# Kernel tuning notes

Measured on AMD Instinct MI355X. Metric: run time of the kernel, lower is better.

Reference implementation:

```python
import jax, jax.numpy as jnp
import numpy as np
import math

B, T, C = 4, 1024, 2048
NH, HS = 16, 128          # n_head, head_size
NLQ, NLKV = 512, 512      # q_latent_dim, kv_latent_dim
DHR = 64                  # rope_head_dim


def setup_inputs() -> dict:
    key = jax.random.key(0)
    ks = jax.random.split(key, 10)
    def w(k, shape, fan_in):
        return jax.random.normal(k, shape, jnp.float32) * (1.0 / math.sqrt(fan_in))
    # RoPE frequencies (standard theta=10000), (T, DHR//2)
    half = DHR // 2
    inv_freq = 1.0 / (10000.0 ** (np.arange(0, half, dtype=np.float32) * 2.0 / DHR))
    ang = np.arange(T, dtype=np.float32)[:, None] * inv_freq[None, :]
    return {
        "x":     jax.random.normal(ks[0], (B, T, C), jnp.float32),
        "W_dq":  w(ks[1], (NLQ, C), C),
        "W_uq":  w(ks[2], (C, NLQ), NLQ),
        "W_dkv": w(ks[3], (NLKV, C), C),
        "W_uk":  w(ks[4], (C, NLKV), NLKV),
        "W_uv":  w(ks[5], (C, NLKV), NLKV),
        "W_o":   w(ks[6], (C, C), C),
        "W_qr":  w(ks[7], (NH * DHR, NLQ), NLQ),
        "W_kr":  w(ks[8], (DHR, C), C),
        "freqs_cos": jnp.asarray(np.cos(ang)),
        "freqs_sin": jnp.asarray(np.sin(ang)),
    }


def _rope(x, cos, sin):
    # x: (B, T, H, D); cos/sin: (T, D//2). Rotate pairs (even, odd).
    b, t, h, d = x.shape
    x_ = x.reshape(b, t, h, d // 2, 2)
    re, im = x_[..., 0], x_[..., 1]
    cos = cos[None, :, None, :]
    sin = sin[None, :, None, :]
    out = jnp.stack([re * cos - im * sin, re * sin + im * cos], axis=-1)
    return out.reshape(b, t, h, d)


def reference(x, W_dq, W_uq, W_dkv, W_uk, W_uv, W_o, W_qr, W_kr, freqs_cos, freqs_sin):
    # Absorbed matrices (training path, rope):
    # k_eff: (nh, nlq, hs) @ (nh, hs, nlkv) -> (nh, nlq, nlkv)
    k_eff = jnp.einsum('hqd,hdk->hqk',
                       W_uq.reshape(NLQ, NH, HS).transpose(1, 0, 2),
                       W_uk.reshape(NH, HS, NLKV))
    # v_eff: (W_uv.T @ W_o.T) -> (nlkv, nh, hs) -> (nh, nlkv, hs)
    v_eff = (W_uv.T @ W_o.T).reshape(NLKV, NH, HS).transpose(1, 0, 2)

    c_kv = x @ W_dkv.T          # (B, T, nlkv)
    c_q = x @ W_dq.T            # (B, T, nlq)

    # content logits: (B, nh, T, T)
    tmp = jnp.einsum('btq,hqk->bhtk', c_q, k_eff)
    attn_c = jnp.einsum('bhtk,bsk->bhts', tmp, c_kv)

    # rope logits
    c_kr = (x @ W_kr.T)[:, :, None, :]                       # (B, T, 1, dhr)
    k_r = _rope(c_kr, freqs_cos, freqs_sin)[:, :, 0, :]      # (B, T, dhr)
    c_qr = (c_q @ W_qr.T).reshape(B, T, NH, DHR)
    q_r = _rope(c_qr, freqs_cos, freqs_sin)                  # (B, T, nh, dhr)
    attn_r = jnp.einsum('bthd,bsd->bhts', q_r, k_r)

    scale = 1.0 / math.sqrt(HS + DHR)
    logits = (attn_c + attn_r) * scale
    causal = jnp.arange(T)[:, None] >= jnp.arange(T)[None, :]
    logits = jnp.where(causal[None, None], logits, -jnp.inf)
    attn = jax.nn.softmax(logits, axis=-1)

    y = jnp.einsum('bhts,bsk->bhtk', attn, c_kv)
    y = jnp.einsum('bhtk,hkd->bthd', y, v_eff).reshape(B, T, C)
    return y
```

## Files before the change

kernel.cpp:

```cpp
#include <hip/hip_runtime.h>
#include <hip/hip_bf16.h>

typedef __attribute__((ext_vector_type(8))) short short8;
typedef __attribute__((ext_vector_type(4))) float f32x4;
typedef __hip_bfloat16 bf16;

#define MFMA16(a,b,c) __builtin_amdgcn_mfma_f32_16x16x32_bf16(a,b,c,0,0,0)

__device__ __forceinline__ void gld_lds16(const void* g, void* l) {
  __builtin_amdgcn_global_load_lds((const __attribute__((address_space(1))) void*)g,
                                   (__attribute__((address_space(3))) void*)l, 16, 0, 0);
}


__global__ __launch_bounds__(256) void cast_bf16_kernel(const float* __restrict__ in,
                                                        bf16* __restrict__ out, long n4) {
  long i = (long)blockIdx.x * blockDim.x + threadIdx.x;
  if (i >= n4) return;
  float4 v = ((const float4*)in)[i];
  union { bf16 b[4]; uint2 u; } p;
  p.b[0] = __float2bfloat16(v.x);
  p.b[1] = __float2bfloat16(v.y);
  p.b[2] = __float2bfloat16(v.z);
  p.b[3] = __float2bfloat16(v.w);
  ((uint2*)out)[i] = p.u;
}

__global__ void transpose_cast_kernel(const float* __restrict__ in, bf16* __restrict__ out,
                                      int R, int C) {
  __shared__ float t[32][33];
  int c0 = blockIdx.x * 32, r0 = blockIdx.y * 32;
  for (int j = threadIdx.y; j < 32; j += 8)
    t[j][threadIdx.x] = in[(long)(r0 + j) * C + c0 + threadIdx.x];
  __syncthreads();
  for (int j = threadIdx.y; j < 32; j += 8)
    out[(long)(c0 + j) * R + r0 + threadIdx.x] = __float2bfloat16(t[threadIdx.x][j]);
}

__global__ __launch_bounds__(256) void rope_q_kernel(const float* __restrict__ in,
                                                     const float* __restrict__ cosT,
                                                     const float* __restrict__ sinT,
                                                     bf16* __restrict__ out, long total) {
  long i = (long)blockIdx.x * blockDim.x + threadIdx.x;
  if (i >= total) return;
  int pair = (int)(i & 31);
  long rest = i >> 5;
  int h = (int)(rest & 15);
  long bt = rest >> 4;
  int t = (int)(bt & 1023);
  long base = (bt * 16 + h) * 64 + pair * 2;
  float re = in[base], im = in[base + 1];
  float c = cosT[t * 32 + pair], s = sinT[t * 32 + pair];
  out[base] = __float2bfloat16(re * c - im * s);
  out[base + 1] = __float2bfloat16(re * s + im * c);
}

__global__ __launch_bounds__(256) void rope_k_kernel(const bf16* __restrict__ ckv_all,
                                                     const float* __restrict__ cosT,
                                                     const float* __restrict__ sinT,
                                                     bf16* __restrict__ out, long total) {
  long i = (long)blockIdx.x * blockDim.x + threadIdx.x;
  if (i >= total) return;
  int pair = (int)(i & 31);
  long bt = i >> 5;
  int t = (int)(bt & 1023);
  const bf16* src = ckv_all + bt * 1088 + 1024 + pair * 2;
  float re = __bfloat162float(src[0]), im = __bfloat162float(src[1]);
  float c = cosT[t * 32 + pair], s = sinT[t * 32 + pair];
  out[bt * 64 + pair * 2] = __float2bfloat16(re * c - im * s);
  out[bt * 64 + pair * 2 + 1] = __float2bfloat16(re * s + im * c);
}

template <int OUT>
__global__ __launch_bounds__(256) void gemm_nt(const bf16* __restrict__ A,
                                               const bf16* __restrict__ B,
                                               void* __restrict__ Cv, int M, int N, int K,
                                               int lda, int ldb, int ldc,
                                               int adiv, int amod, long astr,
                                               int bdiv, int bmod, long bstr, long cstr) {
  __shared__ bf16 As[128 * 32];
  __shared__ bf16 Bs[128 * 32];
  const int tid = threadIdx.x;
  const int lane = tid & 63;
  const int w = tid >> 6;
  const int wr = w >> 1, wc = w & 1;
  const int z = blockIdx.z;
  A += ((long)((z / adiv) % amod)) * astr;
  B += ((long)((z / bdiv) % bmod)) * bstr;
  const int m0 = blockIdx.x * 128, n0 = blockIdx.y * 128;
  const int l16 = lane & 15, lg = lane >> 4;
  const int r0c = tid >> 2, c8 = (tid & 3) * 8;
  f32x4 acc[4][4] = {};
  for (int k0 = 0; k0 < K; k0 += 32) {
    __syncthreads();
    gld_lds16(A + (long)(m0 + r0c) * lda + k0 + c8, &As[tid * 8]);
    gld_lds16(A + (long)(m0 + 64 + r0c) * lda + k0 + c8, &As[2048 + tid * 8]);
    gld_lds16(B + (long)(n0 + r0c) * ldb + k0 + c8, &Bs[tid * 8]);
    gld_lds16(B + (long)(n0 + 64 + r0c) * ldb + k0 + c8, &Bs[2048 + tid * 8]);
    __syncthreads();
    short8 af[4], bfr[4];
#pragma unroll
    for (int i = 0; i < 4; ++i) {
      af[i] = *(const short8*)(&As[(wr * 64 + i * 16 + l16) * 32 + lg * 8]);
      bfr[i] = *(const short8*)(&Bs[(wc * 64 + i * 16 + l16) * 32 + lg * 8]);
    }
#pragma unroll
    for (int i = 0; i < 4; ++i)
#pragma unroll
      for (int j2 = 0; j2 < 4; ++j2) acc[i][j2] = MFMA16(af[i], bfr[j2], acc[i][j2]);
  }
#pragma unroll
  for (int i = 0; i < 4; ++i)
#pragma unroll
    for (int j2 = 0; j2 < 4; ++j2) {
      int col = n0 + wc * 64 + j2 * 16 + l16;
      if (col >= N) continue;
      long rbase = (long)(m0 + wr * 64 + i * 16 + lg * 4);
      for (int r = 0; r < 4; ++r) {
        float v = acc[i][j2][r];
        long idx = (long)z * cstr + (rbase + r) * ldc + col;
        if (OUT == 1) ((bf16*)Cv)[idx] = __float2bfloat16(v);
        else if (OUT == 0) ((float*)Cv)[idx] = v;
        else atomicAdd(&((float*)Cv)[idx], v);
      }
    }
}

__global__ __launch_bounds__(512, 4) void attn_kernel(const bf16* __restrict__ q_h,
                                                      const bf16* __restrict__ q_r,
                                                      const bf16* __restrict__ kh,
                                                      const bf16* __restrict__ kr,
                                                      const bf16* __restrict__ vT,
                                                      float* __restrict__ out) {
  const int x = blockIdx.x, h = blockIdx.y, b = blockIdx.z;
  const int tid = threadIdx.x, lane = tid & 63, w = tid >> 6;
  const int l16 = lane & 15, lg = lane >> 4;
  __shared__ bf16 Klds[2][32 * 192];
  __shared__ bf16 Vlds[2][512 * 8];
  __shared__ bf16 Plds[8][16][40];

  const float sc = 0.0721687836f * 1.44269504f;
  const bf16* vbase = vT + (long)(b * 16 + h) * 131072;
  const int swz = l16 & 7;
  const int vswz = (l16 >> 1) & 3;

  int krow[2], kcs[2];
#pragma unroll
  for (int j = 0; j < 2; ++j) {
    int chunk = tid + 512 * j;
    int row = chunk / 24, c = chunk % 24;
    krow[j] = row & 31;
    kcs[j] = c ^ (row & 7);
  }
  const int vd = tid >> 2, vch = (tid & 3) ^ ((tid >> 3) & 3);

  for (int half = 0; half < 2; ++half) {
    const int q = half ? x : (7 - x);
    const int t0 = q * 128;
    const int rowmin = t0 + w * 16;
    const int nt = (t0 + 128) >> 5;

    short8 aq[6];
    {
      const int trow = t0 + w * 16 + l16;
      const bf16* qhp = q_h + ((long)(b * 1024 + trow)) * 2048 + h * 128;
#pragma unroll
      for (int kk = 0; kk < 4; ++kk) aq[kk] = *(const short8*)(qhp + kk * 32 + lg * 8);
      const bf16* qrp = q_r + (((long)b * 1024 + trow) * 16 + h) * 64;
      aq[4] = *(const short8*)(qrp + lg * 8);
      aq[5] = *(const short8*)(qrp + 32 + lg * 8);
    }

    f32x4 oacc[8] = {};
    float m_run[4], l_run[4];
#pragma unroll
    for (int r = 0; r < 4; ++r) { m_run[r] = -1e30f; l_run[r] = 0.f; }

    const bf16* ksrc[2];
    int kstep[2];
#pragma unroll
    for (int j = 0; j < 2; ++j) {
      if (kcs[j] < 16) { ksrc[j] = kh + ((long)b * 1024 + krow[j]) * 2048 + h * 128 + kcs[j] * 8; kstep[j] = 32 * 2048; }
      else             { ksrc[j] = kr + ((long)b * 1024 + krow[j]) * 64 + (kcs[j] - 16) * 8; kstep[j] = 32 * 64; }
    }
    const bf16* vsrc = vbase + (long)vd * 1024 + vch * 8;

    auto STAGE = [&](int cc) {
      gld_lds16(ksrc[0], &Klds[cc][tid * 8]);
      ksrc[0] += kstep[0];
      if (tid < 256) {
        gld_lds16(ksrc[1], &Klds[cc][(tid + 512) * 8]);
        ksrc[1] += kstep[1];
      }
      gld_lds16(vsrc, &Vlds[cc][tid * 8]);
      vsrc += 32;
    };

    int cur = 0;
    STAGE(0);
    __syncthreads();

    for (int t = 0; t < nt; ++t) {
      if (t + 1 < nt) STAGE(cur ^ 1);
      const int s0 = t * 32;
      if (s0 < rowmin + 16) {
        const bf16* Kb = &Klds[cur][0];
        f32x4 s_acc[2] = {};
#pragma unroll
        for (int kk = 0; kk < 6; ++kk) {
          int u = kk * 4 + lg;
          short8 b0 = *(const short8*)(Kb + l16 * 192 + ((u ^ swz) * 8));
          short8 b1 = *(const short8*)(Kb + (16 + l16) * 192 + ((u ^ swz) * 8));
          s_acc[0] = MFMA16(aq[kk], b0, s_acc[0]);
          s_acc[1] = MFMA16(aq[kk], b1, s_acc[1]);
        }
        const bool need_mask = (s0 + 31 > rowmin);
        float p[2][4], rmax[4];
#pragma unroll
        for (int r = 0; r < 4; ++r) {
          float s0v = s_acc[0][r] * sc, s1v = s_acc[1][r] * sc;
          if (need_mask) {
            int tg = rowmin + lg * 4 + r;
            if (s0 + l16 > tg) s0v = -1e30f;
            if (s0 + 16 + l16 > tg) s1v = -1e30f;
          }
          p[0][r] = s0v; p[1][r] = s1v;
          float mx = fmaxf(s0v, s1v);
          mx = fmaxf(mx, __shfl_xor(mx, 1));
          mx = fmaxf(mx, __shfl_xor(mx, 2));
          mx = fmaxf(mx, __shfl_xor(mx, 4));
          mx = fmaxf(mx, __shfl_xor(mx, 8));
          rmax[r] = mx;
        }
        float need = rmax[0] - m_run[0];
        need = fmaxf(need, rmax[1] - m_run[1]);
        need = fmaxf(need, rmax[2] - m_run[2]);
        need = fmaxf(need, rmax[3] - m_run[3]);
        if (__any(need > 8.0f)) {
          float alpha[4];
#pragma unroll
          for (int r = 0; r < 4; ++r) {
            float mnew = fmaxf(m_run[r], rmax[r]);
            alpha[r] = exp2f(m_run[r] - mnew);
            m_run[r] = mnew;
            l_run[r] *= alpha[r];
          }
#pragma unroll
          for (int f = 0; f < 8; ++f)
#pragma unroll
            for (int r = 0; r < 4; ++r) oacc[f][r] *= alpha[r];
        }
#pragma unroll
        for (int r = 0; r < 4; ++r) {
          float p0 = exp2f(p[0][r] - m_run[r]);
          float p1 = exp2f(p[1][r] - m_run[r]);
          p[0][r] = p0; p[1][r] = p1;
          float rs = p0 + p1;
          rs += __shfl_xor(rs, 1);
          rs += __shfl_xor(rs, 2);
          rs += __shfl_xor(rs, 4);
          rs += __shfl_xor(rs, 8);
          l_run[r] += rs;
        }
#pragma unroll
        for (int nf = 0; nf < 2; ++nf)
#pragma unroll
          for (int r = 0; r < 4; ++r)
            Plds[w][lg * 4 + r][nf * 16 + l16] = __float2bfloat16(p[nf][r]);
        short8 pa = *(const short8*)(&Plds[w][l16][lg * 8]);
        const bf16* Vb = &Vlds[cur][0];
#pragma unroll
        for (int f = 0; f < 8; ++f) {
          int slot = (f * 16 + l16) * 4 + (lg ^ vswz);
          short8 vb = *(const short8*)(Vb + slot * 8);
          oacc[f] = MFMA16(pa, vb, oacc[f]);
        }
      }
      __syncthreads();
      cur ^= 1;
    }

#pragma unroll
    for (int f = 0; f < 8; ++f)
#pragma unroll
      for (int r = 0; r < 4; ++r) {
        int t = t0 + w * 16 + lg * 4 + r;
        int col = f * 16 + l16;
        out[((long)(b * 1024 + t)) * 2048 + h * 128 + col] = oacc[f][r] / l_run[r];
      }
  }
}

extern "C" void kernel_launch(void* const* d_in, const int* in_sizes, int n_in, void* d_out,
                              int out_size, void* d_ws, size_t ws_size, hipStream_t stream) {
  const float* x = (const float*)d_in[0];
  const float* W_dq = (const float*)d_in[1];
  const float* W_uq = (const float*)d_in[2];
  const float* W_dkv = (const float*)d_in[3];
  const float* W_uk = (const float*)d_in[4];
  const float* W_uv = (const float*)d_in[5];
  const float* W_o = (const float*)d_in[6];
  const float* W_qr = (const float*)d_in[7];
  const float* W_kr = (const float*)d_in[8];
  const float* fcos = (const float*)d_in[9];
  const float* fsin = (const float*)d_in[10];
  float* out = (float*)d_out;

  char* p = (char*)d_ws;
  auto alloc = [&](long bytes) { void* r = p; p += (bytes + 255) & ~255L; return r; };
  bf16* xb = (bf16*)alloc(8388608L * 2);
  bf16* Wcat = (bf16*)alloc(1152L * 2048 * 2);
  bf16* Wqr_b = (bf16*)alloc(524288L * 2);
  bf16* Wo_b = (bf16*)alloc(4194304L * 2);
  bf16* Wcat2 = (bf16*)alloc(2097152L * 2);
  bf16* WuvT_b = (bf16*)alloc(1048576L * 2);
  bf16* ckv_all = (bf16*)alloc(4096L * 1088 * 2);
  float* veff_f32 = (float*)alloc(1048576L * 4);
  bf16* veffT_b = (bf16*)alloc(1048576L * 2);
  bf16* q_h = (bf16*)alloc(8388608L * 2);
  bf16* k_h = (bf16*)alloc(8388608L * 2);
  float* c_qr_f = (float*)alloc(4194304L * 4);
  bf16* q_r_b = (bf16*)alloc(4194304L * 2);
  bf16* k_r_b = (bf16*)alloc(262144L * 2);
  bf16* vT_b = (bf16*)alloc(8388608L * 2);
  bf16* WuqT_b = Wcat2;
  bf16* Wuk_b = Wcat2 + 1048576L;

  cast_bf16_kernel<<<8192, 256, 0, stream>>>(x, xb, 2097152);
  cast_bf16_kernel<<<1024, 256, 0, stream>>>(W_dq, Wcat, 262144);
  cast_bf16_kernel<<<1024, 256, 0, stream>>>(W_dkv, Wcat + 512L * 2048, 262144);
  cast_bf16_kernel<<<128, 256, 0, stream>>>(W_kr, Wcat + 1024L * 2048, 32768);
  cast_bf16_kernel<<<512, 256, 0, stream>>>(W_qr, Wqr_b, 131072);
  cast_bf16_kernel<<<4096, 256, 0, stream>>>(W_o, Wo_b, 1048576);
  cast_bf16_kernel<<<1024, 256, 0, stream>>>(W_uk, Wuk_b, 262144);
  transpose_cast_kernel<<<dim3(64, 16), dim3(32, 8), 0, stream>>>(W_uq, WuqT_b, 512, 2048);
  transpose_cast_kernel<<<dim3(16, 64), dim3(32, 8), 0, stream>>>(W_uv, WuvT_b, 2048, 512);
  hipMemsetAsync(veff_f32, 0, 1048576L * 4, stream);

  gemm_nt<1><<<dim3(32, 9, 1), 256, 0, stream>>>(xb, Wcat, ckv_all, 4096, 1088, 2048, 2048, 2048,
                                                 1088, 1, 1, 0, 1, 1, 0, 0);
  gemm_nt<2><<<dim3(16, 4, 4), 256, 0, stream>>>(Wo_b, WuvT_b, veff_f32, 2048, 512, 512, 2048,
                                                 2048, 512, 1, 4, 512, 1, 4, 512, 0);
  cast_bf16_kernel<<<1024, 256, 0, stream>>>(veff_f32, veffT_b, 262144);
  gemm_nt<1><<<dim3(32, 16, 2), 256, 0, stream>>>(ckv_all, Wcat2, q_h, 4096, 2048, 512, 1088,
                                                  512, 2048, 1, 2, 512, 1, 2, 1048576, 8388608);
  gemm_nt<0><<<dim3(32, 8, 1), 256, 0, stream>>>(ckv_all, Wqr_b, c_qr_f, 4096, 1024, 512, 1088,
                                                 512, 1024, 1, 1, 0, 1, 1, 0, 0);
  gemm_nt<1><<<dim3(1, 8, 64), 256, 0, stream>>>(veffT_b, ckv_all + 512, vT_b, 128, 1024, 512,
                                                 512, 1088, 1024, 1, 16, 65536, 16, 4,
                                                 1024L * 1088, 131072);
  rope_q_kernel<<<8192, 256, 0, stream>>>(c_qr_f, fcos, fsin, q_r_b, 2097152);
  rope_k_kernel<<<512, 256, 0, stream>>>(ckv_all, fcos, fsin, k_r_b, 131072);
  attn_kernel<<<dim3(4, 16, 4), 512, 0, stream>>>(q_h, q_r_b, k_h, k_r_b, vT_b, out);
}
```

Baseline: 390.4 us.

## Add 256x256 GEMM for q/k absorption, bf16 c_qr, one query block per attention CTA

Replaces the q_h/k_h absorbed-projection GEMM with a new 256x256-tile, 512-thread bf16 GEMM that gives each wave more output reuse. The c_qr intermediate is now written and read as bf16 instead of fp32, which halves that buffer's traffic at the cost of an extra rounding before RoPE. The attention kernel now launches one CTA per 128-row query block (largest first) instead of pairing a long and a short block in one CTA, which gives more CTAs but a less even amount of work per CTA. The new GEMM has a single LDS buffer with no prefetch and assumes the dimensions divide evenly.

```diff
diff --git a/kernel.cpp b/kernel.cpp
--- a/kernel.cpp
+++ b/kernel.cpp
@@ -37,7 +37,7 @@
     out[(long)(c0 + j) * R + r0 + threadIdx.x] = __float2bfloat16(t[threadIdx.x][j]);
 }
 
-__global__ __launch_bounds__(256) void rope_q_kernel(const float* __restrict__ in,
+__global__ __launch_bounds__(256) void rope_q_kernel(const bf16* __restrict__ in,
                                                      const float* __restrict__ cosT,
                                                      const float* __restrict__ sinT,
                                                      bf16* __restrict__ out, long total) {
@@ -49,7 +49,7 @@
   long bt = rest >> 4;
   int t = (int)(bt & 1023);
   long base = (bt * 16 + h) * 64 + pair * 2;
-  float re = in[base], im = in[base + 1];
+  float re = __bfloat162float(in[base]), im = __bfloat162float(in[base + 1]);
   float c = cosT[t * 32 + pair], s = sinT[t * 32 + pair];
   out[base] = __float2bfloat16(re * c - im * s);
   out[base + 1] = __float2bfloat16(re * s + im * c);
@@ -126,13 +126,68 @@
     }
 }
 
+__global__ __launch_bounds__(512) void gemm256_nt(const bf16* __restrict__ A,
+                                                  const bf16* __restrict__ B,
+                                                  bf16* __restrict__ C, int K,
+                                                  int lda, int ldb, int ldc,
+                                                  long astr, long bstr, long cstr) {
+  __shared__ bf16 As[256 * 32];
+  __shared__ bf16 Bs[256 * 32];
+  const int tid = threadIdx.x;
+  const int lane = tid & 63;
+  const int w = tid >> 6;
+  const int wr = w >> 2, wc = w & 3;
+  const int z = blockIdx.z;
+  A += (long)z * astr;
+  B += (long)z * bstr;
+  C += (long)z * cstr;
+  const int m0 = blockIdx.x * 256, n0 = blockIdx.y * 256;
+  const int l16 = lane & 15, lg = lane >> 4;
+  const int r0 = tid >> 2, c0 = tid & 3;
+  const int cs0 = c0 ^ (r0 & 3);
+  const int r1 = 128 + r0, cs1 = c0 ^ (r1 & 3);
+  const int swz = l16 & 3;
+  f32x4 acc[8][4] = {};
+  for (int k0 = 0; k0 < K; k0 += 32) {
+    __syncthreads();
+    gld_lds16(A + (long)(m0 + r0) * lda + k0 + cs0 * 8, &As[tid * 8]);
+    gld_lds16(A + (long)(m0 + r1) * lda + k0 + cs1 * 8, &As[(tid + 512) * 8]);
+    gld_lds16(B + (long)(n0 + r0) * ldb + k0 + cs0 * 8, &Bs[tid * 8]);
+    gld_lds16(B + (long)(n0 + r1) * ldb + k0 + cs1 * 8, &Bs[(tid + 512) * 8]);
+    __syncthreads();
+    short8 bfr[4];
+#pragma unroll
+    for (int j = 0; j < 4; ++j) {
+      int row = wc * 64 + j * 16 + l16;
+      bfr[j] = *(const short8*)(&Bs[(row * 4 + (lg ^ swz)) * 8]);
+    }
+#pragma unroll
+    for (int i = 0; i < 8; ++i) {
+      int row = wr * 128 + i * 16 + l16;
+      short8 af = *(const short8*)(&As[(row * 4 + (lg ^ swz)) * 8]);
+#pragma unroll
+      for (int j = 0; j < 4; ++j) acc[i][j] = MFMA16(af, bfr[j], acc[i][j]);
+    }
+  }
+#pragma unroll
+  for (int i = 0; i < 8; ++i)
+#pragma unroll
+    for (int j = 0; j < 4; ++j) {
+      int col = n0 + wc * 64 + j * 16 + l16;
+      long rbase = (long)(m0 + wr * 128 + i * 16 + lg * 4);
+#pragma unroll
+      for (int r = 0; r < 4; ++r)
+        C[(rbase + r) * (long)ldc + col] = __float2bfloat16(acc[i][j][r]);
+    }
+}
+
 __global__ __launch_bounds__(512, 4) void attn_kernel(const bf16* __restrict__ q_h,
                                                       const bf16* __restrict__ q_r,
                                                       const bf16* __restrict__ kh,
                                                       const bf16* __restrict__ kr,
                                                       const bf16* __restrict__ vT,
                                                       float* __restrict__ out) {
-  const int x = blockIdx.x, h = blockIdx.y, b = blockIdx.z;
+  const int qb = 7 - blockIdx.x, h = blockIdx.y, b = blockIdx.z;
   const int tid = threadIdx.x, lane = tid & 63, w = tid >> 6;
   const int l16 = lane & 15, lg = lane >> 4;
   __shared__ bf16 Klds[2][32 * 192];
@@ -154,141 +209,138 @@
   }
   const int vd = tid >> 2, vch = (tid & 3) ^ ((tid >> 3) & 3);
 
-  for (int half = 0; half < 2; ++half) {
-    const int q = half ? x : (7 - x);
-    const int t0 = q * 128;
-    const int rowmin = t0 + w * 16;
-    const int nt = (t0 + 128) >> 5;
-
-    short8 aq[6];
-    {
-      const int trow = t0 + w * 16 + l16;
-      const bf16* qhp = q_h + ((long)(b * 1024 + trow)) * 2048 + h * 128;
-#pragma unroll
-      for (int kk = 0; kk < 4; ++kk) aq[kk] = *(const short8*)(qhp + kk * 32 + lg * 8);
-      const bf16* qrp = q_r + (((long)b * 1024 + trow) * 16 + h) * 64;
-      aq[4] = *(const short8*)(qrp + lg * 8);
-      aq[5] = *(const short8*)(qrp + 32 + lg * 8);
-    }
-
-    f32x4 oacc[8] = {};
-    float m_run[4], l_run[4];
-#pragma unroll
-    for (int r = 0; r < 4; ++r) { m_run[r] = -1e30f; l_run[r] = 0.f; }
-
-    const bf16* ksrc[2];
-    int kstep[2];
-#pragma unroll
-    for (int j = 0; j < 2; ++j) {
-      if (kcs[j] < 16) { ksrc[j] = kh + ((long)b * 1024 + krow[j]) * 2048 + h * 128 + kcs[j] * 8; kstep[j] = 32 * 2048; }
-      else             { ksrc[j] = kr + ((long)b * 1024 + krow[j]) * 64 + (kcs[j] - 16) * 8; kstep[j] = 32 * 64; }
-    }
-    const bf16* vsrc = vbase + (long)vd * 1024 + vch * 8;
-
-    auto STAGE = [&](int cc) {
-      gld_lds16(ksrc[0], &Klds[cc][tid * 8]);
-      ksrc[0] += kstep[0];
-      if (tid < 256) {
-        gld_lds16(ksrc[1], &Klds[cc][(tid + 512) * 8]);
-        ksrc[1] += kstep[1];
-      }
-      gld_lds16(vsrc, &Vlds[cc][tid * 8]);
-      vsrc += 32;
-    };
-
-    int cur = 0;
-    STAGE(0);
+  const int t0 = qb * 128;
+  const int rowmin = t0 + w * 16;
+  const int nt = (t0 + 128) >> 5;
+
+  short8 aq[6];
+  {
+    const int trow = t0 + w * 16 + l16;
+    const bf16* qhp = q_h + ((long)(b * 1024 + trow)) * 2048 + h * 128;
+#pragma unroll
+    for (int kk = 0; kk < 4; ++kk) aq[kk] = *(const short8*)(qhp + kk * 32 + lg * 8);
+    const bf16* qrp = q_r + (((long)b * 1024 + trow) * 16 + h) * 64;
+    aq[4] = *(const short8*)(qrp + lg * 8);
+    aq[5] = *(const short8*)(qrp + 32 + lg * 8);
+  }
+
+  f32x4 oacc[8] = {};
+  float m_run[4], l_run[4];
+#pragma unroll
+  for (int r = 0; r < 4; ++r) { m_run[r] = -1e30f; l_run[r] = 0.f; }
+
+  const bf16* ksrc[2];
+  int kstep[2];
+#pragma unroll
+  for (int j = 0; j < 2; ++j) {
+    if (kcs[j] < 16) { ksrc[j] = kh + ((long)b * 1024 + krow[j]) * 2048 + h * 128 + kcs[j] * 8; kstep[j] = 32 * 2048; }
+    else             { ksrc[j] = kr + ((long)b * 1024 + krow[j]) * 64 + (kcs[j] - 16) * 8; kstep[j] = 32 * 64; }
+  }
+  const bf16* vsrc = vbase + (long)vd * 1024 + vch * 8;
+
+  auto STAGE = [&](int cc) {
+    gld_lds16(ksrc[0], &Klds[cc][tid * 8]);
+    ksrc[0] += kstep[0];
+    if (tid < 256) {
+      gld_lds16(ksrc[1], &Klds[cc][(tid + 512) * 8]);
+      ksrc[1] += kstep[1];
+    }
+    gld_lds16(vsrc, &Vlds[cc][tid * 8]);
+    vsrc += 32;
+  };
+
+  int cur = 0;
+  STAGE(0);
+  __syncthreads();
+
+  for (int t = 0; t < nt; ++t) {
+    if (t + 1 < nt) STAGE(cur ^ 1);
+    const int s0 = t * 32;
+    if (s0 < rowmin + 16) {
+      const bf16* Kb = &Klds[cur][0];
+      f32x4 s_acc[2] = {};
+#pragma unroll
+      for (int kk = 0; kk < 6; ++kk) {
+        int u = kk * 4 + lg;
+        short8 b0 = *(const short8*)(Kb + l16 * 192 + ((u ^ swz) * 8));
+        short8 b1 = *(const short8*)(Kb + (16 + l16) * 192 + ((u ^ swz) * 8));
+        s_acc[0] = MFMA16(aq[kk], b0, s_acc[0]);
+        s_acc[1] = MFMA16(aq[kk], b1, s_acc[1]);
+      }
+      const bool need_mask = (s0 + 31 > rowmin);
+      float p[2][4], rmax[4];
+#pragma unroll
+      for (int r = 0; r < 4; ++r) {
+        float s0v = s_acc[0][r] * sc, s1v = s_acc[1][r] * sc;
+        if (need_mask) {
+          int tg = rowmin + lg * 4 + r;
+          if (s0 + l16 > tg) s0v = -1e30f;
+          if (s0 + 16 + l16 > tg) s1v = -1e30f;
+        }
+        p[0][r] = s0v; p[1][r] = s1v;
+        float mx = fmaxf(s0v, s1v);
+        mx = fmaxf(mx, __shfl_xor(mx, 1));
+        mx = fmaxf(mx, __shfl_xor(mx, 2));
+        mx = fmaxf(mx, __shfl_xor(mx, 4));
+        mx = fmaxf(mx, __shfl_xor(mx, 8));
+        rmax[r] = mx;
+      }
+      float need = rmax[0] - m_run[0];
+      need = fmaxf(need, rmax[1] - m_run[1]);
+      need = fmaxf(need, rmax[2] - m_run[2]);
+      need = fmaxf(need, rmax[3] - m_run[3]);
+      if (__any(need > 8.0f)) {
+        float alpha[4];
+#pragma unroll
+        for (int r = 0; r < 4; ++r) {
+          float mnew = fmaxf(m_run[r], rmax[r]);
+          alpha[r] = exp2f(m_run[r] - mnew);
+          m_run[r] = mnew;
+          l_run[r] *= alpha[r];
+        }
+#pragma unroll
+        for (int f = 0; f < 8; ++f)
+#pragma unroll
+          for (int r = 0; r < 4; ++r) oacc[f][r] *= alpha[r];
+      }
+#pragma unroll
+      for (int r = 0; r < 4; ++r) {
+        float p0 = exp2f(p[0][r] - m_run[r]);
+        float p1 = exp2f(p[1][r] - m_run[r]);
+        p[0][r] = p0; p[1][r] = p1;
+        float rs = p0 + p1;
+        rs += __shfl_xor(rs, 1);
+        rs += __shfl_xor(rs, 2);
+        rs += __shfl_xor(rs, 4);
+        rs += __shfl_xor(rs, 8);
+        l_run[r] += rs;
+      }
+#pragma unroll
+      for (int nf = 0; nf < 2; ++nf)
+#pragma unroll
+        for (int r = 0; r < 4; ++r)
+          Plds[w][lg * 4 + r][nf * 16 + l16] = __float2bfloat16(p[nf][r]);
+      short8 pa = *(const short8*)(&Plds[w][l16][lg * 8]);
+      const bf16* Vb = &Vlds[cur][0];
+#pragma unroll
+      for (int f = 0; f < 8; ++f) {
+        int slot = (f * 16 + l16) * 4 + (lg ^ vswz);
+        short8 vb = *(const short8*)(Vb + slot * 8);
+        oacc[f] = MFMA16(pa, vb, oacc[f]);
+      }
+    }
     __syncthreads();
-
-    for (int t = 0; t < nt; ++t) {
-      if (t + 1 < nt) STAGE(cur ^ 1);
-      const int s0 = t * 32;
-      if (s0 < rowmin + 16) {
-        const bf16* Kb = &Klds[cur][0];
-        f32x4 s_acc[2] = {};
-#pragma unroll
-        for (int kk = 0; kk < 6; ++kk) {
-          int u = kk * 4 + lg;
-          short8 b0 = *(const short8*)(Kb + l16 * 192 + ((u ^ swz) * 8));
-          short8 b1 = *(const short8*)(Kb + (16 + l16) * 192 + ((u ^ swz) * 8));
-          s_acc[0] = MFMA16(aq[kk], b0, s_acc[0]);
-          s_acc[1] = MFMA16(aq[kk], b1, s_acc[1]);
-        }
-        const bool need_mask = (s0 + 31 > rowmin);
-        float p[2][4], rmax[4];
-#pragma unroll
-        for (int r = 0; r < 4; ++r) {
-          float s0v = s_acc[0][r] * sc, s1v = s_acc[1][r] * sc;
-          if (need_mask) {
-            int tg = rowmin + lg * 4 + r;
-            if (s0 + l16 > tg) s0v = -1e30f;
-            if (s0 + 16 + l16 > tg) s1v = -1e30f;
-          }
-          p[0][r] = s0v; p[1][r] = s1v;
-          float mx = fmaxf(s0v, s1v);
-          mx = fmaxf(mx, __shfl_xor(mx, 1));
-          mx = fmaxf(mx, __shfl_xor(mx, 2));
-          mx = fmaxf(mx, __shfl_xor(mx, 4));
-          mx = fmaxf(mx, __shfl_xor(mx, 8));
-          rmax[r] = mx;
-        }
-        float need = rmax[0] - m_run[0];
-        need = fmaxf(need, rmax[1] - m_run[1]);
-        need = fmaxf(need, rmax[2] - m_run[2]);
-        need = fmaxf(need, rmax[3] - m_run[3]);
-        if (__any(need > 8.0f)) {
-          float alpha[4];
-#pragma unroll
-          for (int r = 0; r < 4; ++r) {
-            float mnew = fmaxf(m_run[r], rmax[r]);
-            alpha[r] = exp2f(m_run[r] - mnew);
-            m_run[r] = mnew;
-            l_run[r] *= alpha[r];
-          }
-#pragma unroll
-          for (int f = 0; f < 8; ++f)
-#pragma unroll
-            for (int r = 0; r < 4; ++r) oacc[f][r] *= alpha[r];
-        }
-#pragma unroll
-        for (int r = 0; r < 4; ++r) {
-          float p0 = exp2f(p[0][r] - m_run[r]);
-          float p1 = exp2f(p[1][r] - m_run[r]);
-          p[0][r] = p0; p[1][r] = p1;
-          float rs = p0 + p1;
-          rs += __shfl_xor(rs, 1);
-          rs += __shfl_xor(rs, 2);
-          rs += __shfl_xor(rs, 4);
-          rs += __shfl_xor(rs, 8);
-          l_run[r] += rs;
-        }
-#pragma unroll
-        for (int nf = 0; nf < 2; ++nf)
-#pragma unroll
-          for (int r = 0; r < 4; ++r)
-            Plds[w][lg * 4 + r][nf * 16 + l16] = __float2bfloat16(p[nf][r]);
-        short8 pa = *(const short8*)(&Plds[w][l16][lg * 8]);
-        const bf16* Vb = &Vlds[cur][0];
-#pragma unroll
-        for (int f = 0; f < 8; ++f) {
-          int slot = (f * 16 + l16) * 4 + (lg ^ vswz);
-          short8 vb = *(const short8*)(Vb + slot * 8);
-          oacc[f] = MFMA16(pa, vb, oacc[f]);
-        }
-      }
-      __syncthreads();
-      cur ^= 1;
-    }
-
-#pragma unroll
-    for (int f = 0; f < 8; ++f)
-#pragma unroll
-      for (int r = 0; r < 4; ++r) {
-        int t = t0 + w * 16 + lg * 4 + r;
-        int col = f * 16 + l16;
-        out[((long)(b * 1024 + t)) * 2048 + h * 128 + col] = oacc[f][r] / l_run[r];
-      }
-  }
+    cur ^= 1;
+  }
+
+#pragma unroll
+  for (int f = 0; f < 8; ++f)
+#pragma unroll
+    for (int r = 0; r < 4; ++r) {
+      int t = t0 + w * 16 + lg * 4 + r;
+      int col = f * 16 + l16;
+      out[((long)(b * 1024 + t)) * 2048 + h * 128 + col] = oacc[f][r] / l_run[r];
+    }
 }
 
 extern "C" void kernel_launch(void* const* d_in, const int* in_sizes, int n_in, void* d_out,
@@ -319,7 +371,7 @@
   bf16* veffT_b = (bf16*)alloc(1048576L * 2);
   bf16* q_h = (bf16*)alloc(8388608L * 2);
   bf16* k_h = (bf16*)alloc(8388608L * 2);
-  float* c_qr_f = (float*)alloc(4194304L * 4);
+  bf16* c_qr_b = (bf16*)alloc(4194304L * 2);
   bf16* q_r_b = (bf16*)alloc(4194304L * 2);
   bf16* k_r_b = (bf16*)alloc(262144L * 2);
   bf16* vT_b = (bf16*)alloc(8388608L * 2);
@@ -342,14 +394,14 @@
   gemm_nt<2><<<dim3(16, 4, 4), 256, 0, stream>>>(Wo_b, WuvT_b, veff_f32, 2048, 512, 512, 2048,
                                                  2048, 512, 1, 4, 512, 1, 4, 512, 0);
   cast_bf16_kernel<<<1024, 256, 0, stream>>>(veff_f32, veffT_b, 262144);
-  gemm_nt<1><<<dim3(32, 16, 2), 256, 0, stream>>>(ckv_all, Wcat2, q_h, 4096, 2048, 512, 1088,
-                                                  512, 2048, 1, 2, 512, 1, 2, 1048576, 8388608);
-  gemm_nt<0><<<dim3(32, 8, 1), 256, 0, stream>>>(ckv_all, Wqr_b, c_qr_f, 4096, 1024, 512, 1088,
+  gemm256_nt<<<dim3(16, 8, 2), 512, 0, stream>>>(ckv_all, Wcat2, q_h, 512, 1088, 512, 2048,
+                                                 512, 1048576, 8388608);
+  gemm_nt<1><<<dim3(32, 8, 1), 256, 0, stream>>>(ckv_all, Wqr_b, c_qr_b, 4096, 1024, 512, 1088,
                                                  512, 1024, 1, 1, 0, 1, 1, 0, 0);
   gemm_nt<1><<<dim3(1, 8, 64), 256, 0, stream>>>(veffT_b, ckv_all + 512, vT_b, 128, 1024, 512,
                                                  512, 1088, 1024, 1, 16, 65536, 16, 4,
                                                  1024L * 1088, 131072);
-  rope_q_kernel<<<8192, 256, 0, stream>>>(c_qr_f, fcos, fsin, q_r_b, 2097152);
+  rope_q_kernel<<<8192, 256, 0, stream>>>(c_qr_b, fcos, fsin, q_r_b, 2097152);
   rope_k_kernel<<<512, 256, 0, stream>>>(ckv_all, fcos, fsin, k_r_b, 131072);
-  attn_kernel<<<dim3(4, 16, 4), 512, 0, stream>>>(q_h, q_r_b, k_h, k_r_b, vT_b, out);
-}
+  attn_kernel<<<dim3(8, 16, 4), 512, 0, stream>>>(q_h, q_r_b, k_h, k_r_b, vT_b, out);
+}
```

Result: slower. 399.0 us (+2.2%).
